# Kernel optimization log

Measured on AMD Instinct MI355X. Metric: run time of the kernel, lower is better.

The kernel has to match this reference:

```python
import jax, jax.numpy as jnp
import numpy as np

HALF = 16  # num_outputs // 2 with num_features = 32
EPS = 1e-5


def _gmul(Wm, h):
    # Wm: [B,N,M,J], h: [B,M,F] -> [B,N,J*F] (j-major feature layout, matching torch split/cat/bmm)
    B, N = Wm.shape[0], Wm.shape[1]
    return jnp.einsum('bnmj,bmf->bnjf', Wm, h).reshape(B, N, -1)


def _bn(z, g, b):
    # training-mode BatchNorm2d on [R, C, 1, 1] == per-channel norm over rows, biased var
    m = z.mean(axis=0)
    v = z.var(axis=0)
    return g * (z - m) / jnp.sqrt(v + EPS) + b


def _block(W, hx, W_lg, hy, P, wx2x, wy2x, bx, wy2y, wx2y, by, gx, btx, gy, bty):
    B, N, M = P.shape[0], P.shape[1], P.shape[2]
    x2x = _gmul(W, hx).reshape(-1, wx2x.shape[0])
    y2x = _gmul(P, hy).reshape(-1, wy2x.shape[0])
    zx = x2x @ wx2x + y2x @ wy2x + bx
    zx = jnp.concatenate([jax.nn.relu(zx[:, :HALF]), zx[:, HALF:]], axis=1)
    xo = _bn(zx, gx, btx).reshape(B, N, -1)
    y2y = _gmul(W_lg, hy).reshape(-1, wy2y.shape[0])
    x2y = _gmul(jnp.swapaxes(P, 1, 2), hx).reshape(-1, wx2y.shape[0])
    zy = y2y @ wy2y + x2y @ wx2y + by
    zy = jnp.concatenate([jax.nn.relu(zy[:, :HALF]), zy[:, HALF:]], axis=1)
    yo = _bn(zy, gy, bty).reshape(B, M, -1)
    return xo, yo


def _forward(W, x, W_lg, y, P,
             wx2x0, wy2x0, bx0, wy2y0, wx2y0, by0, gx0, btx0, gy0, bty0,
             wx2x_m, wy2x_m, bx_m, wy2y_m, wx2y_m, by_m, gx_m, btx_m, gy_m, bty_m,
             wlx, wly, bl):
    hx, hy = _block(W, x, W_lg, y, P, wx2x0, wy2x0, bx0, wy2y0, wx2y0, by0,
                    gx0, btx0, gy0, bty0)
    for i in range(wx2x_m.shape[0]):  # fixed num_layers loop
        hx, hy = _block(W, hx, W_lg, hy, P,
                        wx2x_m[i], wy2x_m[i], bx_m[i], wy2y_m[i], wx2y_m[i], by_m[i],
                        gx_m[i], btx_m[i], gy_m[i], bty_m[i])
    # final layer: linear only, x branch output
    x2x = _gmul(W, hx).reshape(-1, wlx.shape[0])
    y2x = _gmul(P, hy).reshape(-1, wly.shape[0])
    out = (x2x @ wlx + y2x @ wly + bl).reshape(W.shape[0], W.shape[1], -1)
    return out


def setup_inputs() -> dict:
    key = jax.random.key(0)
    ks = iter(jax.random.split(key, 40))
    B, N, M, J, F, L, C = 1, 2048, 4096, 3, 32, 6, 2
    d = {}
    d['W'] = jax.random.normal(next(ks), (B, N, N, J), jnp.float32)
    d['x'] = jax.random.normal(next(ks), (B, N, 1), jnp.float32)
    d['W_lg'] = jax.random.normal(next(ks), (B, M, M, J), jnp.float32)
    d['y'] = jax.random.normal(next(ks), (B, M, 1), jnp.float32)
    d['P'] = jax.random.normal(next(ks), (B, N, M, 2), jnp.float32)
    s = 0.1
    d['wx2x0'] = jax.random.normal(next(ks), (J * 1, F), jnp.float32) * s
    d['wy2x0'] = jax.random.normal(next(ks), (2 * 1, F), jnp.float32) * s
    d['bx0'] = jax.random.normal(next(ks), (F,), jnp.float32) * s
    d['wy2y0'] = jax.random.normal(next(ks), (J * 1, F), jnp.float32) * s
    d['wx2y0'] = jax.random.normal(next(ks), (2 * 1, F), jnp.float32) * s
    d['by0'] = jax.random.normal(next(ks), (F,), jnp.float32) * s
    d['gx0'] = jnp.ones((F,), jnp.float32)
    d['btx0'] = jnp.zeros((F,), jnp.float32)
    d['gy0'] = jnp.ones((F,), jnp.float32)
    d['bty0'] = jnp.zeros((F,), jnp.float32)
    d['wx2x_m'] = jax.random.normal(next(ks), (L, J * F, F), jnp.float32) * s
    d['wy2x_m'] = jax.random.normal(next(ks), (L, 2 * F, F), jnp.float32) * s
    d['bx_m'] = jax.random.normal(next(ks), (L, F), jnp.float32) * s
    d['wy2y_m'] = jax.random.normal(next(ks), (L, J * F, F), jnp.float32) * s
    d['wx2y_m'] = jax.random.normal(next(ks), (L, 2 * F, F), jnp.float32) * s
    d['by_m'] = jax.random.normal(next(ks), (L, F), jnp.float32) * s
    d['gx_m'] = jnp.ones((L, F), jnp.float32)
    d['btx_m'] = jnp.zeros((L, F), jnp.float32)
    d['gy_m'] = jnp.ones((L, F), jnp.float32)
    d['bty_m'] = jnp.zeros((L, F), jnp.float32)
    d['wlx'] = jax.random.normal(next(ks), (J * F, C), jnp.float32) * s
    d['wly'] = jax.random.normal(next(ks), (2 * F, C), jnp.float32) * s
    d['bl'] = jax.random.normal(next(ks), (C,), jnp.float32) * s
    return d


def reference(W, x, W_lg, y, P,
              wx2x0, wy2x0, bx0, wy2y0, wx2y0, by0, gx0, btx0, gy0, bty0,
              wx2x_m, wy2x_m, bx_m, wy2y_m, wx2y_m, by_m, gx_m, btx_m, gy_m, bty_m,
              wlx, wly, bl):
    return _forward(W, x, W_lg, y, P,
                    wx2x0, wy2x0, bx0, wy2y0, wx2y0, by0, gx0, btx0, gy0, bty0,
                    wx2x_m, wy2x_m, bx_m, wy2y_m, wx2y_m, by_m, gx_m, btx_m, gy_m, bty_m,
                    wlx, wly, bl)
```

## Files before the change

kernel.cpp:

```cpp
#include <hip/hip_runtime.h>

typedef _Float16 f16x8 __attribute__((ext_vector_type(8)));
typedef float f32x4 __attribute__((ext_vector_type(4)));
typedef unsigned short us4v __attribute__((ext_vector_type(4)));

__device__ inline unsigned short f16b(float v) {
    _Float16 h = (_Float16)v;
    return __builtin_bit_cast(unsigned short, h);
}

__device__ inline void atomAddF(float* p, float v) {
    __hip_atomic_fetch_add(p, v, __ATOMIC_RELAXED, __HIP_MEMORY_SCOPE_AGENT);
}

__global__ __launch_bounds__(256) void cvt_all(const float* __restrict__ W, const float* __restrict__ P,
                                               const float* __restrict__ WL,
                                               unsigned short* __restrict__ Wb, unsigned short* __restrict__ Pb,
                                               unsigned short* __restrict__ WLb) {
    int i = blockIdx.x * 256 + threadIdx.x;
    const float* src; unsigned short* dst; int idx;
    if (i < 3145728)               { src = W;  dst = Wb;  idx = i; }
    else if (i < 3145728 + 4194304){ src = P;  dst = Pb;  idx = i - 3145728; }
    else                           { src = WL; dst = WLb; idx = i - (3145728 + 4194304); }
    float4 v = ((const float4*)src)[idx];
    us4v o;
    o[0] = f16b(v.x); o[1] = f16b(v.y); o[2] = f16b(v.z); o[3] = f16b(v.w);
    ((us4v*)dst)[idx] = o;
}

__global__ __launch_bounds__(256) void transpose_p(const float* __restrict__ P,
                                                   unsigned short* __restrict__ PT) {
    __shared__ unsigned int lds[64][33];
    int bid = blockIdx.x;
    int m0 = (bid & 127) * 32;
    int n0 = (bid >> 7) * 64;
    int tid = threadIdx.x;
    const float2* P2 = (const float2*)P;
    #pragma unroll
    for (int it = 0; it < 8; ++it) {
        int idx = it * 256 + tid;
        int nl = idx >> 5, ml = idx & 31;
        float2 v = P2[(size_t)(n0 + nl) * 4096 + (m0 + ml)];
        unsigned int pk = (unsigned int)f16b(v.x) | ((unsigned int)f16b(v.y) << 16);
        lds[nl][ml] = pk;
    }
    __syncthreads();
    unsigned int* PTu = (unsigned int*)PT;
    #pragma unroll
    for (int it = 0; it < 8; ++it) {
        int idx = it * 256 + tid;
        int ml = idx >> 6, nl = idx & 63;
        PTu[(size_t)(m0 + ml) * 2048 + (n0 + nl)] = lds[nl][ml];
    }
}

__global__ __launch_bounds__(256) void build_b(
    const float* __restrict__ srcx, const float* __restrict__ srcy,
    int Fin, int Fout, int buildB2, int use_bn,
    const float* __restrict__ stats,
    const float* __restrict__ gx, const float* __restrict__ btx,
    const float* __restrict__ gy, const float* __restrict__ bty,
    const float* __restrict__ w1a, const float* __restrict__ w1b,
    const float* __restrict__ w2a, const float* __restrict__ w2b,
    unsigned short* __restrict__ B1f, unsigned short* __restrict__ B2f) {
    int tid0 = blockIdx.x * 256 + threadIdx.x;
    const int NB1 = 14336 * 32;
    int isB2 = 0, t2 = tid0;
    if (tid0 >= NB1) {
        if (!buildB2) return;
        isB2 = 1; t2 = tid0 - NB1;
        if (t2 >= 16384 * 32) return;
    }
    int e = t2 & 7, lane = (t2 >> 3) & 63, hh = (t2 >> 9) & 1, t = t2 >> 10;
    int k = (t << 5) | ((lane >> 4) << 3) | e;
    int g = (hh << 4) | (lane & 15);
    float v = 0.f;
    if (g < Fout) {
        const float* hr; const float* wc; int useY;
        if (!isB2) {
            if (k < 6144) { int m = k / 3, j = k - 3 * m; hr = srcx + m * Fin; wc = w1a + (j * Fin) * Fout + g; useY = 0; }
            else { int k2 = k - 6144; int m = k2 >> 1, p = k2 & 1; hr = srcy + m * Fin; wc = w1b + (p * Fin) * Fout + g; useY = 1; }
        } else {
            if (k < 12288) { int m = k / 3, j = k - 3 * m; hr = srcy + m * Fin; wc = w2a + (j * Fin) * Fout + g; useY = 1; }
            else { int k2 = k - 12288; int n = k2 >> 1, p = k2 & 1; hr = srcx + n * Fin; wc = w2b + (p * Fin) * Fout + g; useY = 0; }
        }
        float a = 0.f;
        if (use_bn) {
            const float* st = useY ? stats + 64 : stats;
            const float* gv = useY ? gy : gx;
            const float* bv = useY ? bty : btx;
            float invn = useY ? (1.f / 4096.f) : (1.f / 2048.f);
            #pragma unroll
            for (int f = 0; f < 32; ++f) {
                float mean = st[f] * invn;
                float var = st[32 + f] * invn - mean * mean;
                float sc = gv[f] * rsqrtf(var + 1e-5f);
                float h = sc * (hr[f] - mean) + bv[f];
                a += h * wc[f * Fout];
            }
        } else {
            for (int f = 0; f < Fin; ++f) a += hr[f] * wc[f * Fout];
        }
        v = a;
    }
    if (!isB2) B1f[t2] = f16b(v); else B2f[t2] = f16b(v);
}

__global__ __launch_bounds__(256) void gemm_kernel(
    const unsigned short* __restrict__ Wb, const unsigned short* __restrict__ Pb,
    const unsigned short* __restrict__ WLb, const unsigned short* __restrict__ PTb,
    const unsigned short* __restrict__ B1f, const unsigned short* __restrict__ B2f,
    float* __restrict__ px, float* __restrict__ py, float* __restrict__ stats, int nwgx) {
    int bid = blockIdx.x;
    if (bid == 0 && threadIdx.x < 128) stats[threadIdx.x] = 0.f;
    const unsigned short *A1, *A2, *Bf;
    float* Z;
    int K1, K2len, split, seg, Mbase;
    if (bid < nwgx) {
        A1 = Wb; A2 = Pb; Bf = B1f;
        K1 = 6144; K2len = 8192; split = 6;
        int mwg = bid / 14; seg = bid % 14;
        Mbase = mwg * 128;
        Z = px + (size_t)seg * 65536;
    } else {
        int b2 = bid - nwgx;
        A1 = WLb; A2 = PTb; Bf = B2f;
        K1 = 12288; K2len = 4096; split = 12;
        int mwg = b2 / 16; seg = b2 % 16;
        Mbase = mwg * 128;
        Z = py + (size_t)seg * 131072;
    }
    int wid = threadIdx.x >> 6, lane = threadIdx.x & 63;
    int rowbase = Mbase + wid * 32;
    int kb = seg << 10;
    const unsigned short* Ab; int rowlen, kloc;
    if (seg < split) { Ab = A1; rowlen = K1; kloc = kb; }
    else             { Ab = A2; rowlen = K2len; kloc = kb - K1; }
    const unsigned short* ap0 = Ab + (size_t)(rowbase + (lane & 15)) * rowlen + kloc + ((lane >> 4) << 3);
    const unsigned short* ap1 = ap0 + (size_t)16 * rowlen;
    const unsigned short* bp = Bf + ((size_t)(kb >> 5)) * 1024 + lane * 8;
    f32x4 acc00 = {0.f,0.f,0.f,0.f}, acc01 = {0.f,0.f,0.f,0.f};
    f32x4 acc10 = {0.f,0.f,0.f,0.f}, acc11 = {0.f,0.f,0.f,0.f};
    #pragma unroll 4
    for (int ks = 0; ks < 32; ++ks) {
        f16x8 a0 = *(const f16x8*)ap0;
        f16x8 a1 = *(const f16x8*)ap1;
        f16x8 b0 = *(const f16x8*)bp;
        f16x8 b1 = *(const f16x8*)(bp + 512);
        acc00 = __builtin_amdgcn_mfma_f32_16x16x32_f16(a0, b0, acc00, 0, 0, 0);
        acc10 = __builtin_amdgcn_mfma_f32_16x16x32_f16(a1, b0, acc10, 0, 0, 0);
        acc01 = __builtin_amdgcn_mfma_f32_16x16x32_f16(a0, b1, acc01, 0, 0, 0);
        acc11 = __builtin_amdgcn_mfma_f32_16x16x32_f16(a1, b1, acc11, 0, 0, 0);
        ap0 += 32; ap1 += 32; bp += 1024;
    }
    int col = lane & 15, r0 = (lane >> 4) << 2;
    float* z0 = Z + (size_t)(rowbase + r0) * 32 + col;
    #pragma unroll
    for (int r = 0; r < 4; ++r) {
        z0[(size_t)r * 32]             = acc00[r];
        z0[(size_t)r * 32 + 16]        = acc01[r];
        z0[(size_t)(r + 16) * 32]      = acc10[r];
        z0[(size_t)(r + 16) * 32 + 16] = acc11[r];
    }
}

__global__ __launch_bounds__(256) void reduce_stats(
    const float* __restrict__ px, const float* __restrict__ py,
    const float* __restrict__ bx, const float* __restrict__ by,
    float* __restrict__ zax, float* __restrict__ zay,
    float* __restrict__ stats) {
    __shared__ float lsum[4][8][8];
    int bid = blockIdx.x, tid = threadIdx.x;
    const float4* src; const float* bias; float4* dst; float* st; int nseg, i4, stride4;
    if (bid < 64) { src = (const float4*)px; bias = bx; dst = (float4*)zax; st = stats;      nseg = 14; i4 = bid * 256 + tid;        stride4 = 16384; }
    else          { src = (const float4*)py; bias = by; dst = (float4*)zay; st = stats + 64; nseg = 16; i4 = (bid - 64) * 256 + tid; stride4 = 32768; }
    float4 s = {0.f, 0.f, 0.f, 0.f};
    for (int g = 0; g < nseg; ++g) {
        float4 v = src[(size_t)g * stride4 + i4];
        s.x += v.x; s.y += v.y; s.z += v.z; s.w += v.w;
    }
    int c0 = (i4 & 7) * 4;
    float4 b4 = *(const float4*)(bias + c0);
    s.x += b4.x; s.y += b4.y; s.z += b4.z; s.w += b4.w;
    if (c0 < 16) {
        s.x = fmaxf(s.x, 0.f); s.y = fmaxf(s.y, 0.f);
        s.z = fmaxf(s.z, 0.f); s.w = fmaxf(s.w, 0.f);
    }
    dst[i4] = s;
    float4 s2 = {s.x * s.x, s.y * s.y, s.z * s.z, s.w * s.w};
    #pragma unroll
    for (int mask = 8; mask <= 32; mask <<= 1) {
        s.x += __shfl_xor(s.x, mask); s.y += __shfl_xor(s.y, mask);
        s.z += __shfl_xor(s.z, mask); s.w += __shfl_xor(s.w, mask);
        s2.x += __shfl_xor(s2.x, mask); s2.y += __shfl_xor(s2.y, mask);
        s2.z += __shfl_xor(s2.z, mask); s2.w += __shfl_xor(s2.w, mask);
    }
    int w = tid >> 6, ln = tid & 63;
    if (ln < 8) {
        lsum[w][ln][0] = s.x;  lsum[w][ln][1] = s.y;  lsum[w][ln][2] = s.z;  lsum[w][ln][3] = s.w;
        lsum[w][ln][4] = s2.x; lsum[w][ln][5] = s2.y; lsum[w][ln][6] = s2.z; lsum[w][ln][7] = s2.w;
    }
    __syncthreads();
    if (tid < 64) {
        int q = tid >> 3, e = tid & 7;
        float v = lsum[0][q][e] + lsum[1][q][e] + lsum[2][q][e] + lsum[3][q][e];
        int col = q * 4 + (e & 3);
        atomAddF((e < 4) ? &st[col] : &st[32 + col], v);
    }
}

__global__ __launch_bounds__(256) void out_final(const float* __restrict__ px,
                                                 const float* __restrict__ bl,
                                                 float* __restrict__ out) {
    int tid = blockIdx.x * 256 + threadIdx.x;
    if (tid < 4096) {
        int n = tid >> 1, c = tid & 1;
        float a = bl[c];
        for (int s = 0; s < 14; ++s) a += px[(size_t)s * 65536 + n * 32 + c];
        out[tid] = a;
    }
}

extern "C" void kernel_launch(void* const* d_in, const int* in_sizes, int n_in,
                              void* d_out, int out_size, void* d_ws, size_t ws_size,
                              hipStream_t stream) {
    const float* W    = (const float*)d_in[0];
    const float* x    = (const float*)d_in[1];
    const float* WL   = (const float*)d_in[2];
    const float* y    = (const float*)d_in[3];
    const float* P    = (const float*)d_in[4];
    const float* wx2x0 = (const float*)d_in[5];
    const float* wy2x0 = (const float*)d_in[6];
    const float* bx0   = (const float*)d_in[7];
    const float* wy2y0 = (const float*)d_in[8];
    const float* wx2y0 = (const float*)d_in[9];
    const float* by0   = (const float*)d_in[10];
    const float* gx0   = (const float*)d_in[11];
    const float* btx0  = (const float*)d_in[12];
    const float* gy0   = (const float*)d_in[13];
    const float* bty0  = (const float*)d_in[14];
    const float* wx2x_m = (const float*)d_in[15];
    const float* wy2x_m = (const float*)d_in[16];
    const float* bx_m   = (const float*)d_in[17];
    const float* wy2y_m = (const float*)d_in[18];
    const float* wx2y_m = (const float*)d_in[19];
    const float* by_m   = (const float*)d_in[20];
    const float* gx_m   = (const float*)d_in[21];
    const float* btx_m  = (const float*)d_in[22];
    const float* gy_m   = (const float*)d_in[23];
    const float* bty_m  = (const float*)d_in[24];
    const float* wlx = (const float*)d_in[25];
    const float* wly = (const float*)d_in[26];
    const float* bl  = (const float*)d_in[27];

    char* base = (char*)d_ws;
    unsigned short* Wb  = (unsigned short*)(base + 0);
    unsigned short* Pb  = (unsigned short*)(base + 25165824);
    unsigned short* WLb = (unsigned short*)(base + 58720256);
    unsigned short* PTb = (unsigned short*)(base + 159383552);
    unsigned short* B1f = (unsigned short*)(base + 192937984);
    unsigned short* B2f = (unsigned short*)(base + 193855488);
    float* zax   = (float*)(base + 194904064);
    float* zay   = (float*)(base + 195166208);
    float* stats = (float*)(base + 195690496);
    float* px    = (float*)(base + 195691008);
    float* py    = (float*)(base + 199361024);

    cvt_all<<<77824, 256, 0, stream>>>(W, P, WL, Wb, Pb, WLb);
    transpose_p<<<4096, 256, 0, stream>>>(P, PTb);

    build_b<<<3840, 256, 0, stream>>>(x, y, 1, 32, 1, 0, nullptr, nullptr, nullptr, nullptr, nullptr,
                                      wx2x0, wy2x0, wy2y0, wx2y0, B1f, B2f);
    gemm_kernel<<<736, 256, 0, stream>>>(Wb, Pb, WLb, PTb, B1f, B2f, px, py, stats, 224);
    reduce_stats<<<192, 256, 0, stream>>>(px, py, bx0, by0, zax, zay, stats);

    for (int i = 0; i < 6; ++i) {
        const float* gv  = (i == 0) ? gx0  : gx_m  + (i - 1) * 32;
        const float* bv  = (i == 0) ? btx0 : btx_m + (i - 1) * 32;
        const float* gvy = (i == 0) ? gy0  : gy_m  + (i - 1) * 32;
        const float* bvy = (i == 0) ? bty0 : bty_m + (i - 1) * 32;
        build_b<<<3840, 256, 0, stream>>>(zax, zay, 32, 32, 1, 1, stats, gv, bv, gvy, bvy,
                                          wx2x_m + i * 3072, wy2x_m + i * 2048,
                                          wy2y_m + i * 3072, wx2y_m + i * 2048, B1f, B2f);
        gemm_kernel<<<736, 256, 0, stream>>>(Wb, Pb, WLb, PTb, B1f, B2f, px, py, stats, 224);
        reduce_stats<<<192, 256, 0, stream>>>(px, py, bx_m + i * 32, by_m + i * 32, zax, zay, stats);
    }

    build_b<<<1792, 256, 0, stream>>>(zax, zay, 32, 2, 0, 1, stats,
                                      gx_m + 5 * 32, btx_m + 5 * 32, gy_m + 5 * 32, bty_m + 5 * 32,
                                      wlx, wly, nullptr, nullptr, B1f, B2f);
    gemm_kernel<<<224, 256, 0, stream>>>(Wb, Pb, WLb, PTb, B1f, B2f, px, py, stats, 224);
    out_final<<<16, 256, 0, stream>>>(px, bl, (float*)d_out);
}
```

Before: 710.2 us.

## Fuse fp32-to-fp16 conversion into first GEMM and double K-split count

Removes the standalone conversion kernel. The first layer's GEMM now reads the fp32 W, P and W_lg directly, converts them to fp16 in registers, and writes the fp16 copies back for later layers to reuse. The K-split is also halved in size (512 instead of 1024), which doubles the workgroup count and the number of partial-sum segments, so reduce_stats and out_final now sum twice as many partials. Fusing saves one read of the fp32 matrices, while the extra segments add partial-sum traffic and reduction work.

```diff
diff --git a/kernel.cpp b/kernel.cpp
--- a/kernel.cpp
+++ b/kernel.cpp
@@ -9,23 +9,15 @@
     return __builtin_bit_cast(unsigned short, h);
 }
 
+__device__ inline f16x8 cvt8(float4 a, float4 b) {
+    f16x8 r;
+    r[0] = (_Float16)a.x; r[1] = (_Float16)a.y; r[2] = (_Float16)a.z; r[3] = (_Float16)a.w;
+    r[4] = (_Float16)b.x; r[5] = (_Float16)b.y; r[6] = (_Float16)b.z; r[7] = (_Float16)b.w;
+    return r;
+}
+
 __device__ inline void atomAddF(float* p, float v) {
     __hip_atomic_fetch_add(p, v, __ATOMIC_RELAXED, __HIP_MEMORY_SCOPE_AGENT);
-}
-
-__global__ __launch_bounds__(256) void cvt_all(const float* __restrict__ W, const float* __restrict__ P,
-                                               const float* __restrict__ WL,
-                                               unsigned short* __restrict__ Wb, unsigned short* __restrict__ Pb,
-                                               unsigned short* __restrict__ WLb) {
-    int i = blockIdx.x * 256 + threadIdx.x;
-    const float* src; unsigned short* dst; int idx;
-    if (i < 3145728)               { src = W;  dst = Wb;  idx = i; }
-    else if (i < 3145728 + 4194304){ src = P;  dst = Pb;  idx = i - 3145728; }
-    else                           { src = WL; dst = WLb; idx = i - (3145728 + 4194304); }
-    float4 v = ((const float4*)src)[idx];
-    us4v o;
-    o[0] = f16b(v.x); o[1] = f16b(v.y); o[2] = f16b(v.z); o[3] = f16b(v.w);
-    ((us4v*)dst)[idx] = o;
 }
 
 __global__ __launch_bounds__(256) void transpose_p(const float* __restrict__ P,
@@ -106,52 +98,78 @@
     if (!isB2) B1f[t2] = f16b(v); else B2f[t2] = f16b(v);
 }
 
-__global__ __launch_bounds__(256) void gemm_kernel(
+template<int CVT>
+__global__ __launch_bounds__(256) void gemm_k(
+    const float* __restrict__ Wf, const float* __restrict__ Pf, const float* __restrict__ WLf,
     const unsigned short* __restrict__ Wb, const unsigned short* __restrict__ Pb,
     const unsigned short* __restrict__ WLb, const unsigned short* __restrict__ PTb,
+    unsigned short* __restrict__ Wbw, unsigned short* __restrict__ Pbw, unsigned short* __restrict__ WLbw,
     const unsigned short* __restrict__ B1f, const unsigned short* __restrict__ B2f,
     float* __restrict__ px, float* __restrict__ py, float* __restrict__ stats, int nwgx) {
     int bid = blockIdx.x;
     if (bid == 0 && threadIdx.x < 128) stats[threadIdx.x] = 0.f;
-    const unsigned short *A1, *A2, *Bf;
+    const unsigned short* Bf;
     float* Z;
-    int K1, K2len, split, seg, Mbase;
+    int seg, Mbase, rowlen, kloc, kb, usef32 = 0;
+    const unsigned short* A16; const float* A32; unsigned short* A16w;
     if (bid < nwgx) {
-        A1 = Wb; A2 = Pb; Bf = B1f;
-        K1 = 6144; K2len = 8192; split = 6;
-        int mwg = bid / 14; seg = bid % 14;
+        Bf = B1f;
+        int mwg = bid / 28; seg = bid % 28;
         Mbase = mwg * 128;
+        kb = seg << 9;
         Z = px + (size_t)seg * 65536;
+        if (seg < 12) { rowlen = 6144; kloc = kb;        A16 = Wb; A32 = Wf; A16w = Wbw; usef32 = CVT; }
+        else          { rowlen = 8192; kloc = kb - 6144; A16 = Pb; A32 = Pf; A16w = Pbw; usef32 = CVT; }
     } else {
         int b2 = bid - nwgx;
-        A1 = WLb; A2 = PTb; Bf = B2f;
-        K1 = 12288; K2len = 4096; split = 12;
-        int mwg = b2 / 16; seg = b2 % 16;
+        Bf = B2f;
+        int mwg = b2 / 32; seg = b2 % 32;
         Mbase = mwg * 128;
+        kb = seg << 9;
         Z = py + (size_t)seg * 131072;
+        if (seg < 24) { rowlen = 12288; kloc = kb;         A16 = WLb; A32 = WLf; A16w = WLbw; usef32 = CVT; }
+        else          { rowlen = 4096;  kloc = kb - 12288; A16 = PTb; A32 = nullptr; A16w = nullptr; usef32 = 0; }
     }
     int wid = threadIdx.x >> 6, lane = threadIdx.x & 63;
     int rowbase = Mbase + wid * 32;
-    int kb = seg << 10;
-    const unsigned short* Ab; int rowlen, kloc;
-    if (seg < split) { Ab = A1; rowlen = K1; kloc = kb; }
-    else             { Ab = A2; rowlen = K2len; kloc = kb - K1; }
-    const unsigned short* ap0 = Ab + (size_t)(rowbase + (lane & 15)) * rowlen + kloc + ((lane >> 4) << 3);
-    const unsigned short* ap1 = ap0 + (size_t)16 * rowlen;
+    size_t eoff = (size_t)(rowbase + (lane & 15)) * rowlen + kloc + ((lane >> 4) << 3);
+    size_t eoff1 = eoff + (size_t)16 * rowlen;
     const unsigned short* bp = Bf + ((size_t)(kb >> 5)) * 1024 + lane * 8;
     f32x4 acc00 = {0.f,0.f,0.f,0.f}, acc01 = {0.f,0.f,0.f,0.f};
     f32x4 acc10 = {0.f,0.f,0.f,0.f}, acc11 = {0.f,0.f,0.f,0.f};
-    #pragma unroll 4
-    for (int ks = 0; ks < 32; ++ks) {
-        f16x8 a0 = *(const f16x8*)ap0;
-        f16x8 a1 = *(const f16x8*)ap1;
-        f16x8 b0 = *(const f16x8*)bp;
-        f16x8 b1 = *(const f16x8*)(bp + 512);
-        acc00 = __builtin_amdgcn_mfma_f32_16x16x32_f16(a0, b0, acc00, 0, 0, 0);
-        acc10 = __builtin_amdgcn_mfma_f32_16x16x32_f16(a1, b0, acc10, 0, 0, 0);
-        acc01 = __builtin_amdgcn_mfma_f32_16x16x32_f16(a0, b1, acc01, 0, 0, 0);
-        acc11 = __builtin_amdgcn_mfma_f32_16x16x32_f16(a1, b1, acc11, 0, 0, 0);
-        ap0 += 32; ap1 += 32; bp += 1024;
+    if (CVT && usef32) {
+        const float4* f0 = (const float4*)(A32 + eoff);
+        const float4* f1 = (const float4*)(A32 + eoff1);
+        f16x8* w0 = (f16x8*)(A16w + eoff);
+        f16x8* w1 = (f16x8*)(A16w + eoff1);
+        #pragma unroll 4
+        for (int ks = 0; ks < 16; ++ks) {
+            f16x8 a0 = cvt8(f0[0], f0[1]);
+            f16x8 a1 = cvt8(f1[0], f1[1]);
+            *w0 = a0; *w1 = a1;
+            f16x8 b0 = *(const f16x8*)bp;
+            f16x8 b1 = *(const f16x8*)(bp + 512);
+            acc00 = __builtin_amdgcn_mfma_f32_16x16x32_f16(a0, b0, acc00, 0, 0, 0);
+            acc10 = __builtin_amdgcn_mfma_f32_16x16x32_f16(a1, b0, acc10, 0, 0, 0);
+            acc01 = __builtin_amdgcn_mfma_f32_16x16x32_f16(a0, b1, acc01, 0, 0, 0);
+            acc11 = __builtin_amdgcn_mfma_f32_16x16x32_f16(a1, b1, acc11, 0, 0, 0);
+            f0 += 8; f1 += 8; w0 += 4; w1 += 4; bp += 1024;
+        }
+    } else {
+        const unsigned short* ap0 = A16 + eoff;
+        const unsigned short* ap1 = A16 + eoff1;
+        #pragma unroll 4
+        for (int ks = 0; ks < 16; ++ks) {
+            f16x8 a0 = *(const f16x8*)ap0;
+            f16x8 a1 = *(const f16x8*)ap1;
+            f16x8 b0 = *(const f16x8*)bp;
+            f16x8 b1 = *(const f16x8*)(bp + 512);
+            acc00 = __builtin_amdgcn_mfma_f32_16x16x32_f16(a0, b0, acc00, 0, 0, 0);
+            acc10 = __builtin_amdgcn_mfma_f32_16x16x32_f16(a1, b0, acc10, 0, 0, 0);
+            acc01 = __builtin_amdgcn_mfma_f32_16x16x32_f16(a0, b1, acc01, 0, 0, 0);
+            acc11 = __builtin_amdgcn_mfma_f32_16x16x32_f16(a1, b1, acc11, 0, 0, 0);
+            ap0 += 32; ap1 += 32; bp += 1024;
+        }
     }
     int col = lane & 15, r0 = (lane >> 4) << 2;
     float* z0 = Z + (size_t)(rowbase + r0) * 32 + col;
@@ -172,8 +190,8 @@
     __shared__ float lsum[4][8][8];
     int bid = blockIdx.x, tid = threadIdx.x;
     const float4* src; const float* bias; float4* dst; float* st; int nseg, i4, stride4;
-    if (bid < 64) { src = (const float4*)px; bias = bx; dst = (float4*)zax; st = stats;      nseg = 14; i4 = bid * 256 + tid;        stride4 = 16384; }
-    else          { src = (const float4*)py; bias = by; dst = (float4*)zay; st = stats + 64; nseg = 16; i4 = (bid - 64) * 256 + tid; stride4 = 32768; }
+    if (bid < 64) { src = (const float4*)px; bias = bx; dst = (float4*)zax; st = stats;      nseg = 28; i4 = bid * 256 + tid;        stride4 = 16384; }
+    else          { src = (const float4*)py; bias = by; dst = (float4*)zay; st = stats + 64; nseg = 32; i4 = (bid - 64) * 256 + tid; stride4 = 32768; }
     float4 s = {0.f, 0.f, 0.f, 0.f};
     for (int g = 0; g < nseg; ++g) {
         float4 v = src[(size_t)g * stride4 + i4];
@@ -216,7 +234,7 @@
     if (tid < 4096) {
         int n = tid >> 1, c = tid & 1;
         float a = bl[c];
-        for (int s = 0; s < 14; ++s) a += px[(size_t)s * 65536 + n * 32 + c];
+        for (int s = 0; s < 28; ++s) a += px[(size_t)s * 65536 + n * 32 + c];
         out[tid] = a;
     }
 }
@@ -264,14 +282,14 @@
     float* zay   = (float*)(base + 195166208);
     float* stats = (float*)(base + 195690496);
     float* px    = (float*)(base + 195691008);
-    float* py    = (float*)(base + 199361024);
-
-    cvt_all<<<77824, 256, 0, stream>>>(W, P, WL, Wb, Pb, WLb);
+    float* py    = (float*)(base + 203031040);
+
     transpose_p<<<4096, 256, 0, stream>>>(P, PTb);
 
     build_b<<<3840, 256, 0, stream>>>(x, y, 1, 32, 1, 0, nullptr, nullptr, nullptr, nullptr, nullptr,
                                       wx2x0, wy2x0, wy2y0, wx2y0, B1f, B2f);
-    gemm_kernel<<<736, 256, 0, stream>>>(Wb, Pb, WLb, PTb, B1f, B2f, px, py, stats, 224);
+    gemm_k<1><<<1472, 256, 0, stream>>>(W, P, WL, Wb, Pb, WLb, PTb, Wb, Pb, WLb,
+                                        B1f, B2f, px, py, stats, 448);
     reduce_stats<<<192, 256, 0, stream>>>(px, py, bx0, by0, zax, zay, stats);
 
     for (int i = 0; i < 6; ++i) {
@@ -282,13 +300,17 @@
         build_b<<<3840, 256, 0, stream>>>(zax, zay, 32, 32, 1, 1, stats, gv, bv, gvy, bvy,
                                           wx2x_m + i * 3072, wy2x_m + i * 2048,
                                           wy2y_m + i * 3072, wx2y_m + i * 2048, B1f, B2f);
-        gemm_kernel<<<736, 256, 0, stream>>>(Wb, Pb, WLb, PTb, B1f, B2f, px, py, stats, 224);
+        gemm_k<0><<<1472, 256, 0, stream>>>(nullptr, nullptr, nullptr, Wb, Pb, WLb, PTb,
+                                            nullptr, nullptr, nullptr,
+                                            B1f, B2f, px, py, stats, 448);
         reduce_stats<<<192, 256, 0, stream>>>(px, py, bx_m + i * 32, by_m + i * 32, zax, zay, stats);
     }
 
     build_b<<<1792, 256, 0, stream>>>(zax, zay, 32, 2, 0, 1, stats,
                                       gx_m + 5 * 32, btx_m + 5 * 32, gy_m + 5 * 32, bty_m + 5 * 32,
                                       wlx, wly, nullptr, nullptr, B1f, B2f);
-    gemm_kernel<<<224, 256, 0, stream>>>(Wb, Pb, WLb, PTb, B1f, B2f, px, py, stats, 224);
+    gemm_k<0><<<448, 256, 0, stream>>>(nullptr, nullptr, nullptr, Wb, Pb, WLb, PTb,
+                                       nullptr, nullptr, nullptr,
+                                       B1f, B2f, px, py, stats, 448);
     out_final<<<16, 256, 0, stream>>>(px, bl, (float*)d_out);
 }
```

New measurement: 785.4 us. 10.6% more time.

## Split each GEMM tile's K range across waves and reduce partial sums in LDS

Applied to the files above, without the earlier changes.

Each workgroup now covers 32 rows instead of 128. Its four waves each take a quarter of the 1024-wide K segment, and the partial accumulators are combined through shared memory before one coalesced float4 store. The grid grows fourfold (2944 workgroups) to give more parallelism and memory-level concurrency for this bandwidth-bound skinny GEMM. In exchange it adds an LDS round trip and a barrier per workgroup, and the short 8-step K loop gives less latency hiding per wave.

```diff
diff --git a/kernel.cpp b/kernel.cpp
--- a/kernel.cpp
+++ b/kernel.cpp
@@ -106,43 +106,45 @@
     if (!isB2) B1f[t2] = f16b(v); else B2f[t2] = f16b(v);
 }
 
-__global__ __launch_bounds__(256) void gemm_kernel(
+__global__ __launch_bounds__(256) void gemm_k(
     const unsigned short* __restrict__ Wb, const unsigned short* __restrict__ Pb,
     const unsigned short* __restrict__ WLb, const unsigned short* __restrict__ PTb,
     const unsigned short* __restrict__ B1f, const unsigned short* __restrict__ B2f,
     float* __restrict__ px, float* __restrict__ py, float* __restrict__ stats, int nwgx) {
+    __shared__ float lds[4][1024];
     int bid = blockIdx.x;
     if (bid == 0 && threadIdx.x < 128) stats[threadIdx.x] = 0.f;
-    const unsigned short *A1, *A2, *Bf;
+    const unsigned short* Bf;
     float* Z;
-    int K1, K2len, split, seg, Mbase;
+    int seg, Mbase, rowlen, kloc, kb;
+    const unsigned short* A16;
     if (bid < nwgx) {
-        A1 = Wb; A2 = Pb; Bf = B1f;
-        K1 = 6144; K2len = 8192; split = 6;
+        Bf = B1f;
         int mwg = bid / 14; seg = bid % 14;
-        Mbase = mwg * 128;
+        Mbase = mwg * 32;
+        kb = seg << 10;
         Z = px + (size_t)seg * 65536;
+        if (seg < 6) { rowlen = 6144; kloc = kb;        A16 = Wb; }
+        else         { rowlen = 8192; kloc = kb - 6144; A16 = Pb; }
     } else {
         int b2 = bid - nwgx;
-        A1 = WLb; A2 = PTb; Bf = B2f;
-        K1 = 12288; K2len = 4096; split = 12;
+        Bf = B2f;
         int mwg = b2 / 16; seg = b2 % 16;
-        Mbase = mwg * 128;
+        Mbase = mwg * 32;
+        kb = seg << 10;
         Z = py + (size_t)seg * 131072;
+        if (seg < 12) { rowlen = 12288; kloc = kb;         A16 = WLb; }
+        else          { rowlen = 4096;  kloc = kb - 12288; A16 = PTb; }
     }
     int wid = threadIdx.x >> 6, lane = threadIdx.x & 63;
-    int rowbase = Mbase + wid * 32;
-    int kb = seg << 10;
-    const unsigned short* Ab; int rowlen, kloc;
-    if (seg < split) { Ab = A1; rowlen = K1; kloc = kb; }
-    else             { Ab = A2; rowlen = K2len; kloc = kb - K1; }
-    const unsigned short* ap0 = Ab + (size_t)(rowbase + (lane & 15)) * rowlen + kloc + ((lane >> 4) << 3);
+    int kq = wid << 8;
+    const unsigned short* ap0 = A16 + (size_t)(Mbase + (lane & 15)) * rowlen + kloc + kq + ((lane >> 4) << 3);
     const unsigned short* ap1 = ap0 + (size_t)16 * rowlen;
-    const unsigned short* bp = Bf + ((size_t)(kb >> 5)) * 1024 + lane * 8;
+    const unsigned short* bp = Bf + ((size_t)((kb + kq) >> 5)) * 1024 + lane * 8;
     f32x4 acc00 = {0.f,0.f,0.f,0.f}, acc01 = {0.f,0.f,0.f,0.f};
     f32x4 acc10 = {0.f,0.f,0.f,0.f}, acc11 = {0.f,0.f,0.f,0.f};
-    #pragma unroll 4
-    for (int ks = 0; ks < 32; ++ks) {
+    #pragma unroll
+    for (int ks = 0; ks < 8; ++ks) {
         f16x8 a0 = *(const f16x8*)ap0;
         f16x8 a1 = *(const f16x8*)ap1;
         f16x8 b0 = *(const f16x8*)bp;
@@ -154,14 +156,26 @@
         ap0 += 32; ap1 += 32; bp += 1024;
     }
     int col = lane & 15, r0 = (lane >> 4) << 2;
-    float* z0 = Z + (size_t)(rowbase + r0) * 32 + col;
+    float* l = lds[wid];
     #pragma unroll
     for (int r = 0; r < 4; ++r) {
-        z0[(size_t)r * 32]             = acc00[r];
-        z0[(size_t)r * 32 + 16]        = acc01[r];
-        z0[(size_t)(r + 16) * 32]      = acc10[r];
-        z0[(size_t)(r + 16) * 32 + 16] = acc11[r];
-    }
+        l[(r0 + r) * 32 + col]            = acc00[r];
+        l[(r0 + r) * 32 + col + 16]       = acc01[r];
+        l[(r0 + r + 16) * 32 + col]       = acc10[r];
+        l[(r0 + r + 16) * 32 + col + 16]  = acc11[r];
+    }
+    __syncthreads();
+    int t = threadIdx.x;
+    float4 a = ((const float4*)lds[0])[t];
+    float4 b = ((const float4*)lds[1])[t];
+    float4 c = ((const float4*)lds[2])[t];
+    float4 d = ((const float4*)lds[3])[t];
+    float4 s;
+    s.x = (a.x + b.x) + (c.x + d.x);
+    s.y = (a.y + b.y) + (c.y + d.y);
+    s.z = (a.z + b.z) + (c.z + d.z);
+    s.w = (a.w + b.w) + (c.w + d.w);
+    ((float4*)(Z + (size_t)Mbase * 32))[t] = s;
 }
 
 __global__ __launch_bounds__(256) void reduce_stats(
@@ -271,7 +285,7 @@
 
     build_b<<<3840, 256, 0, stream>>>(x, y, 1, 32, 1, 0, nullptr, nullptr, nullptr, nullptr, nullptr,
                                       wx2x0, wy2x0, wy2y0, wx2y0, B1f, B2f);
-    gemm_kernel<<<736, 256, 0, stream>>>(Wb, Pb, WLb, PTb, B1f, B2f, px, py, stats, 224);
+    gemm_k<<<2944, 256, 0, stream>>>(Wb, Pb, WLb, PTb, B1f, B2f, px, py, stats, 896);
     reduce_stats<<<192, 256, 0, stream>>>(px, py, bx0, by0, zax, zay, stats);
 
     for (int i = 0; i < 6; ++i) {
@@ -282,13 +296,13 @@
         build_b<<<3840, 256, 0, stream>>>(zax, zay, 32, 32, 1, 1, stats, gv, bv, gvy, bvy,
                                           wx2x_m + i * 3072, wy2x_m + i * 2048,
                                           wy2y_m + i * 3072, wx2y_m + i * 2048, B1f, B2f);
-        gemm_kernel<<<736, 256, 0, stream>>>(Wb, Pb, WLb, PTb, B1f, B2f, px, py, stats, 224);
+        gemm_k<<<2944, 256, 0, stream>>>(Wb, Pb, WLb, PTb, B1f, B2f, px, py, stats, 896);
         reduce_stats<<<192, 256, 0, stream>>>(px, py, bx_m + i * 32, by_m + i * 32, zax, zay, stats);
     }
 
     build_b<<<1792, 256, 0, stream>>>(zax, zay, 32, 2, 0, 1, stats,
                                       gx_m + 5 * 32, btx_m + 5 * 32, gy_m + 5 * 32, bty_m + 5 * 32,
                                       wlx, wly, nullptr, nullptr, B1f, B2f);
-    gemm_kernel<<<224, 256, 0, stream>>>(Wb, Pb, WLb, PTb, B1f, B2f, px, py, stats, 224);
+    gemm_k<<<896, 256, 0, stream>>>(Wb, Pb, WLb, PTb, B1f, B2f, px, py, stats, 896);
     out_final<<<16, 256, 0, stream>>>(px, bl, (float*)d_out);
 }
```

Measured after the change: 707.8 us. About the same (-0.3%).
